# Kernel optimization log

Measured on AMD Instinct MI355X. Metric: run time of the kernel, lower is better.

Reference implementation:

```python
import jax, jax.numpy as jnp
import numpy as np

N = 20000        # atoms
NEIGH = 12       # neighbors per atom
BSTEPS = 40      # bond GBF steps, range [0, 8]
ASTEPS = 20      # angle GBF steps, range [-1, 1]
H = 64           # hidden size
NCLS = 2         # n_classification
NCRYS = 20       # crystals (contiguous blocks of 1000 atoms)
NREL = 3         # edge relation types


def gbf(data, dmin, dmax, steps):
    # Gaussian basis expansion: exp(-(d - mu)^2 / gamma^2), gamma = (max-min)/steps
    filters = jnp.linspace(dmin, dmax, steps)
    gamma = (dmax - dmin) / steps
    return jnp.exp(-((data[..., None] - filters) ** 2) / gamma ** 2)


def rgcn(x, src, dst, etype, W_rel, W_root, b):
    # RGCNConv (PyG default): out = x @ W_root + b + sum_r mean_{j in N_r(i)} x_j @ W_r
    out = x @ W_root + b
    for r in range(NREL):
        w = (etype == r).astype(x.dtype)                     # [E]
        msg = (x @ W_rel[r])[src] * w[:, None]               # transform-then-gather: [E, H]
        s = jax.ops.segment_sum(msg, dst, num_segments=x.shape[0])
        c = jax.ops.segment_sum(w, dst, num_segments=x.shape[0])
        out = out + s / jnp.maximum(c, 1.0)[:, None]
    return out


def _forward(bond_fea, angle_fea, species, nbr_idx, crys_idx,
             W1b_rel, W1b_root, b1b, W1a_rel, W1a_root, b1a,
             W2b_rel, W2b_root, b2b, W2a_rel, W2a_root, b2a,
             fc_W, fc_b):
    n = bond_fea.shape[0]
    src = jnp.repeat(jnp.arange(n, dtype=jnp.int32), NEIGH)  # edge sources
    dst = nbr_idx.reshape(-1)                                # edge targets
    etype = species[src] + species[dst]                      # 0/1/2 per species pair

    edge_fea = gbf(bond_fea, 0.0, 8.0, BSTEPS).reshape(n, -1)      # [N, 480]
    ang_fea = gbf(angle_fea, -1.0, 1.0, ASTEPS).reshape(n, -1)     # [N, 2880]

    bf = jax.nn.relu(rgcn(edge_fea, src, dst, etype, W1b_rel, W1b_root, b1b))
    af = jax.nn.relu(rgcn(ang_fea, src, dst, etype, W1a_rel, W1a_root, b1a))
    # dropout treated as identity (eval/deterministic reference)
    bf = jax.nn.relu(rgcn(bf, src, dst, etype, W2b_rel, W2b_root, b2b))
    af = jax.nn.relu(rgcn(af, src, dst, etype, W2a_rel, W2a_root, b2a))

    feat = jnp.concatenate([bf, af], axis=1)                 # [N, 128]

    # pool: mean over contiguous [start, end) ranges per crystal
    starts = crys_idx[:, 0]
    crys_id = jnp.searchsorted(starts, jnp.arange(n), side='right') - 1
    sums = jax.ops.segment_sum(feat, crys_id, num_segments=NCRYS)
    counts = (crys_idx[:, 1] - crys_idx[:, 0]).astype(feat.dtype)[:, None]
    pooled = sums / counts                                   # [NCRYS, 128]

    return pooled @ fc_W + fc_b                              # [NCRYS, NCLS]


def setup_inputs() -> dict:
    key = jax.random.key(0)
    ks = jax.random.split(key, 20)
    bond_fea = jax.random.uniform(ks[0], (N, NEIGH), dtype=jnp.float32) * 8.0
    angle_fea = jax.random.uniform(ks[1], (N, NEIGH, NEIGH), dtype=jnp.float32) * 2.0 - 1.0
    species = jax.random.randint(ks[2], (N,), 0, 2, dtype=jnp.int32)
    nbr_idx = jax.random.randint(ks[3], (N, NEIGH), 0, N, dtype=jnp.int32)
    starts = jnp.arange(NCRYS, dtype=jnp.int32) * (N // NCRYS)
    crys_idx = jnp.stack([starts, starts + (N // NCRYS)], axis=1)

    def w(k, shape, fan_in):
        return jax.random.normal(k, shape, dtype=jnp.float32) / np.sqrt(fan_in)

    in_b = BSTEPS * NEIGH            # 480
    in_a = ASTEPS * NEIGH * NEIGH    # 2880
    return {
        'bond_fea': bond_fea, 'angle_fea': angle_fea, 'species': species,
        'nbr_idx': nbr_idx, 'crys_idx': crys_idx,
        'W1b_rel': w(ks[4], (NREL, in_b, H), in_b), 'W1b_root': w(ks[5], (in_b, H), in_b),
        'b1b': jnp.zeros((H,), jnp.float32),
        'W1a_rel': w(ks[6], (NREL, in_a, H), in_a), 'W1a_root': w(ks[7], (in_a, H), in_a),
        'b1a': jnp.zeros((H,), jnp.float32),
        'W2b_rel': w(ks[8], (NREL, H, H), H), 'W2b_root': w(ks[9], (H, H), H),
        'b2b': jnp.zeros((H,), jnp.float32),
        'W2a_rel': w(ks[10], (NREL, H, H), H), 'W2a_root': w(ks[11], (H, H), H),
        'b2a': jnp.zeros((H,), jnp.float32),
        'fc_W': w(ks[12], (2 * H, NCLS), 2 * H), 'fc_b': jnp.zeros((NCLS,), jnp.float32),
    }


def reference(bond_fea, angle_fea, species, nbr_idx, crys_idx,
              W1b_rel, W1b_root, b1b, W1a_rel, W1a_root, b1a,
              W2b_rel, W2b_root, b2b, W2a_rel, W2a_root, b2a,
              fc_W, fc_b):
    return _forward(bond_fea, angle_fea, species, nbr_idx, crys_idx,
                    W1b_rel, W1b_root, b1b, W1a_rel, W1a_root, b1a,
                    W2b_rel, W2b_root, b2b, W2a_rel, W2a_root, b2a,
                    fc_W, fc_b)
```

## Files before the change

kernel.cpp:

```cpp
#include <hip/hip_runtime.h>

#define NN 20000
#define NNP 20096
#define NEIGH 12
#define NCRYS 20
#define MT2 1256
#define NSUB 16

typedef __bf16 bf16x8 __attribute__((ext_vector_type(8)));
typedef __bf16 bf16x4 __attribute__((ext_vector_type(4)));
typedef float f32x4 __attribute__((ext_vector_type(4)));

__device__ __forceinline__ void pack_one(const float* Wrel, const float* Wroot,
                                         __bf16* Wp, int K, int idx) {
    int k = idx >> 8, n = idx & 255;
    int r = n >> 6, h = n & 63;
    float v = (r < 3) ? Wrel[((size_t)r * K + k) * 64 + h] : Wroot[(size_t)k * 64 + h];
    int kt = k >> 5, k8 = (k >> 3) & 3, j = k & 7, nt = n >> 4, ni = n & 15;
    Wp[((((size_t)kt * 16 + nt) * 4 + k8) * 16 + ni) * 8 + j] = (__bf16)v;
}

__global__ __launch_bounds__(256) void setup_kernel(
    const int* __restrict__ species, const int* __restrict__ nbr,
    int* __restrict__ adj, int* __restrict__ deg,
    const float* __restrict__ W1b_rel, const float* __restrict__ W1b_root,
    const float* __restrict__ W1a_rel, const float* __restrict__ W1a_root,
    const float* __restrict__ W2b_rel, const float* __restrict__ W2b_root,
    const float* __restrict__ W2a_rel, const float* __restrict__ W2a_root,
    __bf16* __restrict__ Wp1b, __bf16* __restrict__ Wp1a,
    __bf16* __restrict__ Wp2b, __bf16* __restrict__ Wp2a,
    const float* __restrict__ bond, const float* __restrict__ angle,
    float* __restrict__ bondT, float* __restrict__ angleT) {
    __shared__ float ls[64 * 145];
    const int bx = blockIdx.x, tid = threadIdx.x;
    if (bx < 938) {
        int e = bx * 256 + tid;
        if (e < NN * NEIGH) {
            int i = e / NEIGH;
            int d = nbr[e];
            int r = species[i] + species[d];
            int slot = atomicAdd(&deg[d], 1);
            if (slot < 64) adj[(size_t)d * 64 + slot] = i | (r << 28);
        }
    } else if (bx < 938 + 256) {
        const int S0 = 480 * 256, S1 = S0 + 2880 * 256, S2 = S1 + 64 * 256, S3 = S2 + 64 * 256;
        for (int idx = (bx - 938) * 256 + tid; idx < S3; idx += 256 * 256) {
            if (idx < S0)       pack_one(W1b_rel, W1b_root, Wp1b, 480, idx);
            else if (idx < S1)  pack_one(W1a_rel, W1a_root, Wp1a, 2880, idx - S0);
            else if (idx < S2)  pack_one(W2b_rel, W2b_root, Wp2b, 64, idx - S1);
            else                pack_one(W2a_rel, W2a_root, Wp2a, 64, idx - S2);
        }
    } else {
        int tb = bx - 1194;
        if (tb < 314) {
            int m0 = tb * 64;
            for (int idx = tid; idx < 64 * 144; idx += 256) {
                int mm = idx / 144, j = idx - mm * 144;
                int m = m0 + mm;
                ls[mm * 145 + j] = (m < NN) ? angle[(size_t)m * 144 + j] : 0.f;
            }
            __syncthreads();
            for (int idx = tid; idx < 144 * 64; idx += 256) {
                int j = idx >> 6, mm = idx & 63;
                angleT[(size_t)j * NNP + m0 + mm] = ls[mm * 145 + j];
            }
        } else {
            int m0 = (tb - 314) * 64;
            for (int idx = tid; idx < 64 * 12; idx += 256) {
                int mm = idx / 12, j = idx - mm * 12;
                int m = m0 + mm;
                ls[mm * 13 + j] = (m < NN) ? bond[(size_t)m * 12 + j] : 0.f;
            }
            __syncthreads();
            for (int idx = tid; idx < 12 * 64; idx += 256) {
                int j = idx >> 6, mm = idx & 63;
                bondT[(size_t)j * NNP + m0 + mm] = ls[mm * 13 + j];
            }
        }
    }
}

template <int MODE>
__device__ __forceinline__ void gemm1_body(const float* __restrict__ xT,
                                           const __bf16* __restrict__ Wp,
                                           float* __restrict__ Y, int mb,
                                           __bf16* __restrict__ Al) {
    constexpr int KTOT = (MODE == 0) ? 480 : 2880;
    constexpr int NKT = KTOT / 32;
    constexpr int DIVN = (MODE == 0) ? 40 : 20;
    constexpr float F0 = (MODE == 0) ? 0.f : -1.f;
    constexpr float FS = (MODE == 0) ? (8.f / 39.f) : (2.f / 19.f);
    constexpr float NG2 = ((MODE == 0) ? -25.f : -100.f) * 1.44269504f;
    const float C  = __builtin_amdgcn_exp2f(2.f * NG2 * FS * FS);
    const float P1 = NG2 * FS * FS;
    const float P2 = -2.f * NG2 * FS;

    const int tid = threadIdx.x;
    const int lane = tid & 63, wv = tid >> 6;
    const int m0 = mb * 64;
    const int smt = tid >> 7;
    const int sk8 = (tid >> 5) & 3;
    const int smi = (tid >> 1) & 15;
    const int sjh = (tid & 1) * 4;
    const int sgm = m0 + smt * 16 + smi;
    const int kk0 = sk8 * 8 + sjh;
    const int swoff = (((smt * 4 + sk8) * 16 + smi) * 8 + sjh);
    const int k8b = lane >> 4, nib = lane & 15;
    const bf16x8* Bg = (const bf16x8*)Wp;

    f32x4 acc[4][2] = {};
    bf16x8 bcur[2], bnx[2], bnx2[2];

    auto bload = [&](int kt, bf16x8* d) {
#pragma unroll
        for (int jf = 0; jf < 2; ++jf)
            d[jf] = Bg[(((size_t)kt * 16 + 2 * wv + jf) * 4 + k8b) * 16 + nib];
    };
    auto aload = [&](int kt) -> float {
        int k = kt * 32 + kk0;
        int jr = k / DIVN;
        return xT[(size_t)jr * NNP + sgm];
    };
    auto stage = [&](int kt, float a, __bf16* dst) {
        int k = kt * 32 + kk0;
        int jr = k / DIVN;
        int s = k - jr * DIVN;
        float d0 = a - (F0 + (float)s * FS);
        float e0 = __builtin_amdgcn_exp2f(NG2 * d0 * d0);
        float q0 = __builtin_amdgcn_exp2f(fmaf(P2, d0, P1));
        float e1 = e0 * q0;
        float q1 = q0 * C;
        float e2 = e1 * q1;
        float e3 = e2 * q1 * C;
        bf16x4 vals;
        vals[0] = (__bf16)e0; vals[1] = (__bf16)e1;
        vals[2] = (__bf16)e2; vals[3] = (__bf16)e3;
        *(bf16x4*)&dst[swoff] = vals;
    };

    {
        float a0 = aload(0);
        stage(0, a0, Al);
    }
    float anext = aload(1 < NKT ? 1 : 0);
    bload(0, bcur);
    bload(1 < NKT ? 1 : 0, bnx);
    __syncthreads();

    for (int kt = 0; kt < NKT; ++kt) {
        __bf16* Ab = Al + ((kt & 1) << 11);
        __bf16* An = Al + (((kt & 1) ^ 1) << 11);
        const int ktp2 = (kt + 2 < NKT) ? kt + 2 : NKT - 1;
        bload(ktp2, bnx2);
        float afut = (kt + 2 < NKT) ? aload(kt + 2) : anext;
        bf16x8 af[4];
#pragma unroll
        for (int t = 0; t < 4; ++t)
            af[t] = *(const bf16x8*)&Ab[((((t << 2) + k8b) << 4) + nib) << 3];
#pragma unroll
        for (int i = 0; i < 4; ++i)
#pragma unroll
            for (int j = 0; j < 2; ++j)
                acc[i][j] = __builtin_amdgcn_mfma_f32_16x16x32_bf16(af[i], bcur[j], acc[i][j], 0, 0, 0);
        if (kt + 1 < NKT)
            stage(kt + 1, anext, An);
        __syncthreads();
#pragma unroll
        for (int j = 0; j < 2; ++j) { bcur[j] = bnx[j]; bnx[j] = bnx2[j]; }
        anext = afut;
    }

    const int mrow0 = m0 + ((lane >> 4) << 2);
    const int ncol = (wv << 5) + nib;
#pragma unroll
    for (int i = 0; i < 4; ++i)
#pragma unroll
        for (int j = 0; j < 2; ++j)
#pragma unroll
            for (int v = 0; v < 4; ++v) {
                int m = mrow0 + i * 16 + v;
                if (m < NN) Y[(size_t)m * 256 + ncol + j * 16] = acc[i][j][v];
            }
}

__global__ __launch_bounds__(512, 4) void mega_gemm1(const float* __restrict__ bondT,
                                                     const float* __restrict__ angleT,
                                                     const __bf16* __restrict__ Wp1b,
                                                     const __bf16* __restrict__ Wp1a,
                                                     float* __restrict__ Yb, float* __restrict__ Ya) {
    __shared__ __align__(16) __bf16 Al[2 * 2048];
    int bx = blockIdx.x;
    if (bx < 314) gemm1_body<1>(angleT, Wp1a, Ya, bx, Al);
    else          gemm1_body<0>(bondT, Wp1b, Yb, bx - 314, Al);
}

__global__ __launch_bounds__(256) void mega_gemm2(const __bf16* __restrict__ Hbp,
                                                  const __bf16* __restrict__ Hap,
                                                  const __bf16* __restrict__ Wp2b,
                                                  const __bf16* __restrict__ Wp2a,
                                                  float* __restrict__ Yb, float* __restrict__ Ya) {
    __shared__ __align__(16) __bf16 Al[4096];
    __shared__ __align__(16) __bf16 Bl[4096];
    const int ch = blockIdx.x & 1;
    const int mb = blockIdx.x >> 1;
    const int nb = blockIdx.y;
    const __bf16* Ap = ch ? Hap : Hbp;
    const __bf16* Wp = ch ? Wp2a : Wp2b;
    float* Y = ch ? Ya : Yb;
    const int tid = threadIdx.x;
    const int lane = tid & 63, wv = tid >> 6;
    const int m0 = mb * 128;
    const int rw = wv & 1, cw = wv >> 1;
    f32x4 acc[4][4] = {};
#pragma unroll
    for (int kt = 0; kt < 2; ++kt) {
        __syncthreads();
        {
            const float4* src = (const float4*)(Wp + (((size_t)kt * 16 + nb * 8) << 9));
            float4* dst = (float4*)Bl;
            float4 v0 = src[tid], v1 = src[tid + 256];
            dst[tid] = v0;
            dst[tid + 256] = v1;
        }
        {
            const float4* src = (const float4*)(Ap + (((size_t)kt * MT2 + mb * 8) << 9));
            float4* dst = (float4*)Al;
            float4 v0 = src[tid], v1 = src[tid + 256];
            dst[tid] = v0;
            dst[tid + 256] = v1;
        }
        __syncthreads();
        bf16x8 af[4], bfr[4];
        int fro = ((lane >> 4) << 4) + (lane & 15);
#pragma unroll
        for (int t4 = 0; t4 < 4; ++t4) {
            af[t4] = *(const bf16x8*)&Al[((((rw * 4 + t4) << 6) + fro) << 3)];
            bfr[t4] = *(const bf16x8*)&Bl[((((cw * 4 + t4) << 6) + fro) << 3)];
        }
#pragma unroll
        for (int i = 0; i < 4; ++i)
#pragma unroll
            for (int j = 0; j < 4; ++j)
                acc[i][j] = __builtin_amdgcn_mfma_f32_16x16x32_bf16(af[i], bfr[j], acc[i][j], 0, 0, 0);
    }
    const int n0 = nb * 128 + cw * 64;
    const int mrow0 = m0 + rw * 64 + ((lane >> 4) << 2);
    const int ncol = n0 + (lane & 15);
#pragma unroll
    for (int i = 0; i < 4; ++i)
#pragma unroll
        for (int j = 0; j < 4; ++j)
#pragma unroll
            for (int v = 0; v < 4; ++v) {
                int m = mrow0 + i * 16 + v;
                if (m < NN) Y[(size_t)m * 256 + ncol + j * 16] = acc[i][j][v];
            }
}

__device__ __forceinline__ float agg_node(const float* __restrict__ Y,
                                          const int* __restrict__ adj,
                                          const int* __restrict__ deg,
                                          const float* __restrict__ bias,
                                          int node, int h) {
    int dg = min(deg[node], 64);
    int e = adj[(size_t)node * 64 + h];
    bool val = h < dg;
    int r = e >> 28;
    unsigned long long bl0 = __ballot(val && r == 0);
    unsigned long long bl1 = __ballot(val && r == 1);
    unsigned long long bl2 = __ballot(val && r == 2);
    int c0 = __popcll(bl0), c1 = __popcll(bl1), c2 = __popcll(bl2);
    float s0 = 0.f, s1 = 0.f, s2 = 0.f;
    if (dg > 0) {
        int e0 = __builtin_amdgcn_readfirstlane(e);
        int ec = val ? e : e0;
        for (int k0 = 0; k0 < dg; k0 += 16) {
            float v[16];
#pragma unroll
            for (int i = 0; i < 16; ++i) {
                int ek = __builtin_amdgcn_readlane(ec, k0 + i);
                v[i] = Y[(size_t)(ek & 0x0FFFFFFF) * 256 + (ek >> 28) * 64 + h];
            }
#pragma unroll
            for (int i = 0; i < 16; ++i) {
                int kk = k0 + i;
                if (kk < dg) {
                    int rr = __builtin_amdgcn_readlane(ec, kk) >> 28;
                    if (rr == 0) s0 += v[i];
                    else if (rr == 1) s1 += v[i];
                    else s2 += v[i];
                }
            }
        }
    }
    float o = Y[(size_t)node * 256 + 192 + h] + bias[h] +
              s0 / fmaxf((float)c0, 1.f) + s1 / fmaxf((float)c1, 1.f) +
              s2 / fmaxf((float)c2, 1.f);
    return fmaxf(o, 0.f);
}

__global__ __launch_bounds__(256) void agg_packed(const float* __restrict__ Yb,
                                                  const float* __restrict__ Ya,
                                                  const int* __restrict__ adj,
                                                  const int* __restrict__ deg,
                                                  const float* __restrict__ biasb,
                                                  const float* __restrict__ biasa,
                                                  __bf16* __restrict__ outb,
                                                  __bf16* __restrict__ outa) {
    const float* Y = blockIdx.y ? Ya : Yb;
    const float* bias = blockIdx.y ? biasa : biasb;
    __bf16* outp = blockIdx.y ? outa : outb;
    int node = blockIdx.x * 4 + (threadIdx.x >> 6);
    int h = threadIdx.x & 63;
    float o = (node < NN) ? agg_node(Y, adj, deg, bias, node, h) : 0.f;
    int mt = node >> 4, mi = node & 15;
    int ktt = h >> 5, k8 = (h >> 3) & 3, j = h & 7;
    outp[((((size_t)ktt * MT2 + mt) * 4 + k8) * 16 + mi) * 8 + j] = (__bf16)o;
}

__global__ __launch_bounds__(256) void agg_pool(const float* __restrict__ Yb,
                                                const float* __restrict__ Ya,
                                                const int* __restrict__ adj,
                                                const int* __restrict__ deg,
                                                const float* __restrict__ biasb,
                                                const float* __restrict__ biasa,
                                                const int* __restrict__ crys,
                                                float* __restrict__ pooled) {
    const float* Y = blockIdx.y ? Ya : Yb;
    const float* bias = blockIdx.y ? biasa : biasb;
    const int base = blockIdx.y ? 64 : 0;
    int node = blockIdx.x * 4 + (threadIdx.x >> 6);
    int h = threadIdx.x & 63;
    if (node >= NN) return;
    float o = agg_node(Y, adj, deg, bias, node, h);
    int c = 0;
#pragma unroll
    for (int t = 1; t < NCRYS; ++t) c += (node >= crys[t * 2]) ? 1 : 0;
    int sub = blockIdx.x & (NSUB - 1);
    atomicAdd(&pooled[((size_t)c * NSUB + sub) * 128 + base + h], o);
}

__global__ void final2(const float* __restrict__ pooled, const int* __restrict__ crys,
                       const float* __restrict__ fcW, const float* __restrict__ fcb,
                       float* __restrict__ out) {
    int c = blockIdx.x >> 1, o = blockIdx.x & 1;
    int l = threadIdx.x;
    float cnt = (float)(crys[c * 2 + 1] - crys[c * 2]);
    float sb = 0.f, sa = 0.f;
    for (int s = 0; s < NSUB; ++s) {
        sb += pooled[((size_t)c * NSUB + s) * 128 + l];
        sa += pooled[((size_t)c * NSUB + s) * 128 + 64 + l];
    }
    float a = sb * fcW[l * 2 + o] + sa * fcW[(64 + l) * 2 + o];
    for (int s = 32; s > 0; s >>= 1) a += __shfl_down(a, s);
    if (l == 0) out[c * 2 + o] = a / cnt + fcb[o];
}

extern "C" void kernel_launch(void* const* d_in, const int* in_sizes, int n_in,
                              void* d_out, int out_size, void* d_ws, size_t ws_size,
                              hipStream_t stream) {
    const float* bond    = (const float*)d_in[0];
    const float* angle   = (const float*)d_in[1];
    const int*   species = (const int*)d_in[2];
    const int*   nbr     = (const int*)d_in[3];
    const int*   crys    = (const int*)d_in[4];
    const float* W1b_rel = (const float*)d_in[5];
    const float* W1b_root= (const float*)d_in[6];
    const float* b1b     = (const float*)d_in[7];
    const float* W1a_rel = (const float*)d_in[8];
    const float* W1a_root= (const float*)d_in[9];
    const float* b1a     = (const float*)d_in[10];
    const float* W2b_rel = (const float*)d_in[11];
    const float* W2b_root= (const float*)d_in[12];
    const float* b2b     = (const float*)d_in[13];
    const float* W2a_rel = (const float*)d_in[14];
    const float* W2a_root= (const float*)d_in[15];
    const float* b2a     = (const float*)d_in[16];
    const float* fcW     = (const float*)d_in[17];
    const float* fcb     = (const float*)d_in[18];
    float* out = (float*)d_out;

    char* ws = (char*)d_ws;
    size_t off = 0;
    auto alloc = [&](size_t bytes) {
        char* p = ws + off;
        off = (off + bytes + 255) & ~(size_t)255;
        return p;
    };
    __bf16* Wp1b = (__bf16*)alloc((size_t)480 * 256 * 2);
    __bf16* Wp1a = (__bf16*)alloc((size_t)2880 * 256 * 2);
    __bf16* Wp2b = (__bf16*)alloc((size_t)64 * 256 * 2);
    __bf16* Wp2a = (__bf16*)alloc((size_t)64 * 256 * 2);
    float*  bondT = (float*)alloc((size_t)12 * NNP * 4);
    float*  angleT= (float*)alloc((size_t)144 * NNP * 4);
    float*  Yb   = (float*)alloc((size_t)NN * 256 * 4);
    float*  Ya   = (float*)alloc((size_t)NN * 256 * 4);
    __bf16* Hbp  = (__bf16*)alloc((size_t)2 * MT2 * 512 * 2);
    __bf16* Hap  = (__bf16*)alloc((size_t)2 * MT2 * 512 * 2);
    int*    adj  = (int*)alloc((size_t)NN * 64 * 4);
    int*    deg  = (int*)alloc((size_t)NN * 4);
    float*  pooled = (float*)alloc((size_t)NCRYS * NSUB * 128 * 4);

    hipMemsetAsync(deg, 0, (size_t)NN * 4, stream);
    hipMemsetAsync(pooled, 0, (size_t)NCRYS * NSUB * 128 * 4, stream);

    setup_kernel<<<1822, 256, 0, stream>>>(species, nbr, adj, deg,
                                           W1b_rel, W1b_root, W1a_rel, W1a_root,
                                           W2b_rel, W2b_root, W2a_rel, W2a_root,
                                           Wp1b, Wp1a, Wp2b, Wp2a,
                                           bond, angle, bondT, angleT);

    mega_gemm1<<<628, 512, 0, stream>>>(bondT, angleT, Wp1b, Wp1a, Yb, Ya);
    agg_packed<<<dim3(5024, 2), 256, 0, stream>>>(Yb, Ya, adj, deg, b1b, b1a, Hbp, Hap);
    mega_gemm2<<<dim3(314, 2), 256, 0, stream>>>(Hbp, Hap, Wp2b, Wp2a, Yb, Ya);
    agg_pool<<<dim3(5000, 2), 256, 0, stream>>>(Yb, Ya, adj, deg, b2b, b2a, crys, pooled);
    final2<<<NCRYS * 2, 64, 0, stream>>>(pooled, crys, fcW, fcb, out);
}
```

Measured before the change: 254.3 us.

## Process two K-tiles per barrier phase in the fused GBF GEMM1

The GEMM1 main loop now covers 64 K values per phase instead of 32. It double-buffers a larger LDS tile, so there are half as many __syncthreads barriers and the MFMA work between them doubles. The bond path's K is padded from 480 to 512 so it divides evenly, with zero-memset padding on the weights and the transposed bond features. Divisions in the A staging are replaced by incremental index counters, and the exp math is vectorised over pairs. The trade-offs are more LDS per block, a shorter B-prefetch distance, and extra memsets plus wasted padded work.

```diff
diff --git a/kernel.cpp b/kernel.cpp
--- a/kernel.cpp
+++ b/kernel.cpp
@@ -10,6 +10,7 @@
 typedef __bf16 bf16x8 __attribute__((ext_vector_type(8)));
 typedef __bf16 bf16x4 __attribute__((ext_vector_type(4)));
 typedef float f32x4 __attribute__((ext_vector_type(4)));
+typedef float f32x2 __attribute__((ext_vector_type(2)));
 
 __device__ __forceinline__ void pack_one(const float* Wrel, const float* Wroot,
                                          __bf16* Wp, int K, int idx) {
@@ -85,9 +86,11 @@
                                            const __bf16* __restrict__ Wp,
                                            float* __restrict__ Y, int mb,
                                            __bf16* __restrict__ Al) {
-    constexpr int KTOT = (MODE == 0) ? 480 : 2880;
-    constexpr int NKT = KTOT / 32;
+    constexpr int KTOT = (MODE == 0) ? 512 : 2880;
+    constexpr int NPH = KTOT / 64;
     constexpr int DIVN = (MODE == 0) ? 40 : 20;
+    constexpr int ADDJ = 64 / DIVN;
+    constexpr int ADDS = 64 % DIVN;
     constexpr float F0 = (MODE == 0) ? 0.f : -1.f;
     constexpr float FS = (MODE == 0) ? (8.f / 39.f) : (2.f / 19.f);
     constexpr float NG2 = ((MODE == 0) ? -25.f : -100.f) * 1.44269504f;
@@ -109,65 +112,86 @@
     const bf16x8* Bg = (const bf16x8*)Wp;
 
     f32x4 acc[4][2] = {};
-    bf16x8 bcur[2], bnx[2], bnx2[2];
-
-    auto bload = [&](int kt, bf16x8* d) {
-#pragma unroll
-        for (int jf = 0; jf < 2; ++jf)
-            d[jf] = Bg[(((size_t)kt * 16 + 2 * wv + jf) * 4 + k8b) * 16 + nib];
+    bf16x8 bcur[4];
+
+    int jr0 = kk0 / DIVN,        s0 = kk0 % DIVN;
+    int jr1 = (32 + kk0) / DIVN, s1 = (32 + kk0) % DIVN;
+
+    auto bload = [&](int ph) {
+#pragma unroll
+        for (int jf = 0; jf < 4; ++jf)
+            bcur[jf] = Bg[(((size_t)(2 * ph + (jf >> 1)) * 16 + 2 * wv + (jf & 1)) * 4 + k8b) * 16 + nib];
     };
-    auto aload = [&](int kt) -> float {
-        int k = kt * 32 + kk0;
-        int jr = k / DIVN;
-        return xT[(size_t)jr * NNP + sgm];
+    auto advance = [&]() {
+        jr0 += ADDJ; s0 += ADDS; if (s0 >= DIVN) { s0 -= DIVN; ++jr0; }
+        jr1 += ADDJ; s1 += ADDS; if (s1 >= DIVN) { s1 -= DIVN; ++jr1; }
     };
-    auto stage = [&](int kt, float a, __bf16* dst) {
-        int k = kt * 32 + kk0;
-        int jr = k / DIVN;
-        int s = k - jr * DIVN;
-        float d0 = a - (F0 + (float)s * FS);
-        float e0 = __builtin_amdgcn_exp2f(NG2 * d0 * d0);
-        float q0 = __builtin_amdgcn_exp2f(fmaf(P2, d0, P1));
-        float e1 = e0 * q0;
-        float q1 = q0 * C;
-        float e2 = e1 * q1;
-        float e3 = e2 * q1 * C;
-        bf16x4 vals;
-        vals[0] = (__bf16)e0; vals[1] = (__bf16)e1;
-        vals[2] = (__bf16)e2; vals[3] = (__bf16)e3;
-        *(bf16x4*)&dst[swoff] = vals;
+    auto stage = [&](float a0, float a1, __bf16* dst) {
+        f32x2 d;
+        d.x = a0 - (F0 + (float)s0 * FS);
+        d.y = a1 - (F0 + (float)s1 * FS);
+        f32x2 t = d * d;
+        f32x2 argE = t * NG2;
+        f32x2 argQ = d * P2 + P1;
+        f32x2 e0, q0;
+        e0.x = __builtin_amdgcn_exp2f(argE.x);
+        e0.y = __builtin_amdgcn_exp2f(argE.y);
+        q0.x = __builtin_amdgcn_exp2f(argQ.x);
+        q0.y = __builtin_amdgcn_exp2f(argQ.y);
+        f32x2 e1 = e0 * q0;
+        f32x2 q1 = q0 * C;
+        f32x2 e2 = e1 * q1;
+        f32x2 e3 = e2 * (q1 * C);
+        bf16x4 v0, v1;
+        v0[0] = (__bf16)e0.x; v0[1] = (__bf16)e1.x; v0[2] = (__bf16)e2.x; v0[3] = (__bf16)e3.x;
+        v1[0] = (__bf16)e0.y; v1[1] = (__bf16)e1.y; v1[2] = (__bf16)e2.y; v1[3] = (__bf16)e3.y;
+        *(bf16x4*)&dst[swoff] = v0;
+        *(bf16x4*)&dst[2048 + swoff] = v1;
     };
 
     {
-        float a0 = aload(0);
-        stage(0, a0, Al);
-    }
-    float anext = aload(1 < NKT ? 1 : 0);
-    bload(0, bcur);
-    bload(1 < NKT ? 1 : 0, bnx);
+        float a0 = xT[(size_t)jr0 * NNP + sgm];
+        float a1 = xT[(size_t)jr1 * NNP + sgm];
+        stage(a0, a1, Al);
+        advance();
+    }
+    float an0 = xT[(size_t)jr0 * NNP + sgm];
+    float an1 = xT[(size_t)jr1 * NNP + sgm];
+    bload(0);
     __syncthreads();
 
-    for (int kt = 0; kt < NKT; ++kt) {
-        __bf16* Ab = Al + ((kt & 1) << 11);
-        __bf16* An = Al + (((kt & 1) ^ 1) << 11);
-        const int ktp2 = (kt + 2 < NKT) ? kt + 2 : NKT - 1;
-        bload(ktp2, bnx2);
-        float afut = (kt + 2 < NKT) ? aload(kt + 2) : anext;
+    int cur = 0;
+    for (int ph = 0; ph < NPH; ++ph) {
+        const __bf16* Ab = Al + (cur << 12);
         bf16x8 af[4];
 #pragma unroll
-        for (int t = 0; t < 4; ++t)
-            af[t] = *(const bf16x8*)&Ab[((((t << 2) + k8b) << 4) + nib) << 3];
-#pragma unroll
-        for (int i = 0; i < 4; ++i)
-#pragma unroll
-            for (int j = 0; j < 2; ++j)
-                acc[i][j] = __builtin_amdgcn_mfma_f32_16x16x32_bf16(af[i], bcur[j], acc[i][j], 0, 0, 0);
-        if (kt + 1 < NKT)
-            stage(kt + 1, anext, An);
+        for (int t4 = 0; t4 < 4; ++t4)
+            af[t4] = *(const bf16x8*)&Ab[((((t4 << 2) + k8b) << 4) + nib) << 3];
+#pragma unroll
+        for (int i = 0; i < 4; ++i) {
+            acc[i][0] = __builtin_amdgcn_mfma_f32_16x16x32_bf16(af[i], bcur[0], acc[i][0], 0, 0, 0);
+            acc[i][1] = __builtin_amdgcn_mfma_f32_16x16x32_bf16(af[i], bcur[1], acc[i][1], 0, 0, 0);
+        }
+        bf16x8 ag[4];
+#pragma unroll
+        for (int t4 = 0; t4 < 4; ++t4)
+            ag[t4] = *(const bf16x8*)&Ab[2048 + (((((t4 << 2) + k8b) << 4) + nib) << 3)];
+#pragma unroll
+        for (int i = 0; i < 4; ++i) {
+            acc[i][0] = __builtin_amdgcn_mfma_f32_16x16x32_bf16(ag[i], bcur[2], acc[i][0], 0, 0, 0);
+            acc[i][1] = __builtin_amdgcn_mfma_f32_16x16x32_bf16(ag[i], bcur[3], acc[i][1], 0, 0, 0);
+        }
+        if (ph + 1 < NPH) {
+            bload(ph + 1);
+            stage(an0, an1, Al + ((cur ^ 1) << 12));
+            advance();
+            if (ph + 2 < NPH) {
+                an0 = xT[(size_t)jr0 * NNP + sgm];
+                an1 = xT[(size_t)jr1 * NNP + sgm];
+            }
+        }
         __syncthreads();
-#pragma unroll
-        for (int j = 0; j < 2; ++j) { bcur[j] = bnx[j]; bnx[j] = bnx2[j]; }
-        anext = afut;
+        cur ^= 1;
     }
 
     const int mrow0 = m0 + ((lane >> 4) << 2);
@@ -188,7 +212,7 @@
                                                      const __bf16* __restrict__ Wp1b,
                                                      const __bf16* __restrict__ Wp1a,
                                                      float* __restrict__ Yb, float* __restrict__ Ya) {
-    __shared__ __align__(16) __bf16 Al[2 * 2048];
+    __shared__ __align__(16) __bf16 Al[2 * 4096];
     int bx = blockIdx.x;
     if (bx < 314) gemm1_body<1>(angleT, Wp1a, Ya, bx, Al);
     else          gemm1_body<0>(bondT, Wp1b, Yb, bx - 314, Al);
@@ -387,11 +411,11 @@
         off = (off + bytes + 255) & ~(size_t)255;
         return p;
     };
-    __bf16* Wp1b = (__bf16*)alloc((size_t)480 * 256 * 2);
+    __bf16* Wp1b = (__bf16*)alloc((size_t)512 * 256 * 2);
     __bf16* Wp1a = (__bf16*)alloc((size_t)2880 * 256 * 2);
     __bf16* Wp2b = (__bf16*)alloc((size_t)64 * 256 * 2);
     __bf16* Wp2a = (__bf16*)alloc((size_t)64 * 256 * 2);
-    float*  bondT = (float*)alloc((size_t)12 * NNP * 4);
+    float*  bondT = (float*)alloc((size_t)16 * NNP * 4);
     float*  angleT= (float*)alloc((size_t)144 * NNP * 4);
     float*  Yb   = (float*)alloc((size_t)NN * 256 * 4);
     float*  Ya   = (float*)alloc((size_t)NN * 256 * 4);
@@ -403,6 +427,8 @@
 
     hipMemsetAsync(deg, 0, (size_t)NN * 4, stream);
     hipMemsetAsync(pooled, 0, (size_t)NCRYS * NSUB * 128 * 4, stream);
+    hipMemsetAsync(Wp1b, 0, (size_t)512 * 256 * 2, stream);
+    hipMemsetAsync(bondT, 0, (size_t)16 * NNP * 4, stream);
 
     setup_kernel<<<1822, 256, 0, stream>>>(species, nbr, adj, deg,
                                            W1b_rel, W1b_root, W1a_rel, W1a_root,
```

After: 261.1 us. 1.03x slower.
